# Optimization experiments

Hardware: AMD Instinct MI355X
Metric: run time of the kernel (lower is better)

## Reference

```python
import jax, jax.numpy as jnp
import numpy as np

LATENT = 1024
TEXT = 768
HEADS = 16
HEAD_DIM = LATENT // HEADS
SCALE = HEAD_DIM ** -0.5
LN_EPS = 1e-5


def setup_inputs() -> dict:
    key = jax.random.key(0)
    ks = jax.random.split(key, 16)
    B, Tx, Txf = 4, 4096, 256
    def lin(k, fan_in, fan_out):
        bound = 1.0 / np.sqrt(fan_in)
        kw, kb = jax.random.split(k)
        W = jax.random.uniform(kw, (fan_in, fan_out), jnp.float32, -bound, bound)
        b = jax.random.uniform(kb, (fan_out,), jnp.float32, -bound, bound)
        return W, b
    Wq, bq = lin(ks[0], LATENT, LATENT)
    Wk, bk = lin(ks[1], TEXT, LATENT)
    Wv, bv = lin(ks[2], TEXT, LATENT)
    Wo, bo = lin(ks[3], LATENT, LATENT)
    W1, b1 = lin(ks[4], LATENT, 4 * LATENT)
    W2, b2 = lin(ks[5], 4 * LATENT, LATENT)
    return {
        "x": jax.random.normal(ks[6], (B, Tx, LATENT), jnp.float32),
        "xf": jax.random.normal(ks[7], (B, Txf, TEXT), jnp.float32),
        "Wq": Wq, "bq": bq, "Wk": Wk, "bk": bk, "Wv": Wv, "bv": bv,
        "Wo": Wo, "bo": bo,
        "ln_g": jnp.ones((LATENT,), jnp.float32),
        "ln_b": jnp.zeros((LATENT,), jnp.float32),
        "W1": W1, "b1": b1, "W2": W2, "b2": b2,
    }


def reference(x, xf, Wq, bq, Wk, bk, Wv, bv, Wo, bo, ln_g, ln_b, W1, b1, W2, b2):
    B, Tx, D = x.shape
    Txf = xf.shape[1]
    # projections -> [B, H, T, Dh]
    q = (x @ Wq + bq).reshape(B, Tx, HEADS, HEAD_DIM).transpose(0, 2, 1, 3)
    k = (xf @ Wk + bk).reshape(B, Txf, HEADS, HEAD_DIM).transpose(0, 2, 1, 3)
    v = (xf @ Wv + bv).reshape(B, Txf, HEADS, HEAD_DIM).transpose(0, 2, 1, 3)
    # chunked loop in original == full softmax over keys (dropout=0 at eval)
    scores = jnp.einsum('bhqd,bhkd->bhqk', q * SCALE, k)
    probs = jax.nn.softmax(scores, axis=-1)
    attn = jnp.einsum('bhqk,bhkd->bhqd', probs, v)
    out = attn.transpose(0, 2, 1, 3).reshape(B, Tx, D)
    out = out @ Wo + bo
    # FFN: LayerNorm -> Linear -> GELU(exact) -> Linear
    mu = jnp.mean(out, axis=-1, keepdims=True)
    var = jnp.var(out, axis=-1, keepdims=True)
    h = (out - mu) * jax.lax.rsqrt(var + LN_EPS) * ln_g + ln_b
    h = jax.nn.gelu(h @ W1 + b1, approximate=False)
    ffn = h @ W2 + b2
    out = out + ffn
    return x + out
```

## Files before the change

### kernel.cpp

```cpp
#include <hip/hip_runtime.h>
#include <hip/hip_bf16.h>
#include <cmath>

typedef __bf16 bf16_t;
typedef __bf16 bf16x8 __attribute__((ext_vector_type(8)));
typedef __bf16 bf16x4 __attribute__((ext_vector_type(4)));
typedef float f32x4 __attribute__((ext_vector_type(4)));

#define LATENT 1024
#define HEADS 16
#define HD 64
#define TX 4096
#define TXF 256
#define SCALE_ATTN 0.125f

static __device__ __forceinline__ float b2f(bf16_t b) { return (float)b; }
static __device__ __forceinline__ bf16_t f2b(float f) { return (bf16_t)f; }

static __device__ __forceinline__ void glds16(const bf16_t* g, bf16_t* l) {
    __builtin_amdgcn_global_load_lds(
        (const __attribute__((address_space(1))) void*)g,
        (__attribute__((address_space(3))) void*)l, 16, 0, 0);
}

#define MFMA16(a, b, c) __builtin_amdgcn_mfma_f32_16x16x32_bf16(a, b, c, 0, 0, 0)

__global__ __launch_bounds__(256) void cvt_k(const float* __restrict__ in,
                                             bf16_t* __restrict__ out, long n4) {
    long i = (long)blockIdx.x * 256 + threadIdx.x;
    long stride = (long)gridDim.x * 256;
    for (; i < n4; i += stride) {
        float4 v = ((const float4*)in)[i];
        bf16x4 o;
        o[0] = f2b(v.x); o[1] = f2b(v.y); o[2] = f2b(v.z); o[3] = f2b(v.w);
        *(bf16x4*)&out[i * 4] = o;
    }
}

__global__ __launch_bounds__(256) void tr6_k(
    const float* __restrict__ s0, bf16_t* __restrict__ d0,
    const float* __restrict__ s1, bf16_t* __restrict__ d1,
    const float* __restrict__ s2, bf16_t* __restrict__ d2,
    const float* __restrict__ s3, bf16_t* __restrict__ d3,
    const float* __restrict__ s4, bf16_t* __restrict__ d4,
    const float* __restrict__ s5, bf16_t* __restrict__ d5) {
    int id = blockIdx.x;
    const float* src; bf16_t* dst; int R, C, bx, by;
    if (id < 1024)      { src = s0; dst = d0; R = 1024; C = 1024; bx = id & 31;  by = id >> 5; }
    else if (id < 1792) { id -= 1024; src = s1; dst = d1; R = 768;  C = 1024; bx = id & 31;  by = id >> 5; }
    else if (id < 2560) { id -= 1792; src = s2; dst = d2; R = 768;  C = 1024; bx = id & 31;  by = id >> 5; }
    else if (id < 3584) { id -= 2560; src = s3; dst = d3; R = 1024; C = 1024; bx = id & 31;  by = id >> 5; }
    else if (id < 7680) { id -= 3584; src = s4; dst = d4; R = 1024; C = 4096; bx = id & 127; by = id >> 7; }
    else                { id -= 7680; src = s5; dst = d5; R = 4096; C = 1024; bx = id & 31;  by = id >> 5; }
    __shared__ float t[32][33];
    int x = threadIdx.x & 31, y0 = threadIdx.x >> 5;
    for (int i = 0; i < 32; i += 8)
        t[y0 + i][x] = src[(long)(by * 32 + y0 + i) * C + bx * 32 + x];
    __syncthreads();
    for (int i = 0; i < 32; i += 8)
        dst[(long)(bx * 32 + y0 + i) * R + by * 32 + x] = f2b(t[x][y0 + i]);
}

template <int EPI>
__global__ __launch_bounds__(256, 2) void gemm_k(
    const bf16_t* __restrict__ A, const bf16_t* __restrict__ Bt,
    const float* __restrict__ bias, void* __restrict__ C,
    const bf16_t* __restrict__ resb16, const float* __restrict__ resf32,
    int M, int N, int K) {
    __shared__ __align__(16) bf16_t As[128 * 64];
    __shared__ __align__(16) bf16_t Bs[128 * 64];
    int tid = threadIdx.x;
    int lane = tid & 63, wid = tid >> 6;
    int quad = lane >> 4, l16 = lane & 15;
    int wm = wid >> 1, wn = wid & 1;
    int srow0 = wid * 8 + (lane >> 3);
    int schunk = (lane & 7) ^ (lane >> 3);

    int nwg = gridDim.x * gridDim.y;
    int wgid = blockIdx.y * gridDim.x + blockIdx.x;
    int cpx = nwg >> 3;
    int swz = (wgid & 7) * cpx + (wgid >> 3);
    long bm = swz % gridDim.x;
    long bn = swz / gridDim.x;

    f32x4 acc[4][4] = {};
    const bf16_t* Ab = A + (bm * 128 + srow0) * (long)K + schunk * 8;
    const bf16_t* Bb = Bt + (bn * 128 + srow0) * (long)K + schunk * 8;
    bf16_t* AsD = As + wid * 512;
    bf16_t* BsD = Bs + wid * 512;

    for (int k0 = 0; k0 < K; k0 += 64) {
        __syncthreads();
#pragma unroll
        for (int t = 0; t < 4; t++) {
            glds16(Ab + k0 + (long)t * 32 * K, AsD + t * 2048);
            glds16(Bb + k0 + (long)t * 32 * K, BsD + t * 2048);
        }
        __syncthreads();
#pragma unroll
        for (int s = 0; s < 2; s++) {
            bf16x8 af[4], bfr[4];
#pragma unroll
            for (int mi = 0; mi < 4; mi++) {
                int r = wm * 64 + mi * 16 + l16;
                af[mi] = *(const bf16x8*)&As[r * 64 + (((s * 4 + quad) ^ (r & 7)) * 8)];
            }
#pragma unroll
            for (int ni = 0; ni < 4; ni++) {
                int r = wn * 64 + ni * 16 + l16;
                bfr[ni] = *(const bf16x8*)&Bs[r * 64 + (((s * 4 + quad) ^ (r & 7)) * 8)];
            }
#pragma unroll
            for (int mi = 0; mi < 4; mi++)
#pragma unroll
                for (int ni = 0; ni < 4; ni++)
                    acc[mi][ni] = MFMA16(af[mi], bfr[ni], acc[mi][ni]);
        }
    }

    int colb = (int)bn * 128 + wn * 64;
    float bvv[4];
#pragma unroll
    for (int ni = 0; ni < 4; ni++) bvv[ni] = bias[colb + ni * 16 + l16];
#pragma unroll
    for (int mi = 0; mi < 4; mi++) {
        long grow = bm * 128 + wm * 64 + mi * 16 + quad * 4;
#pragma unroll
        for (int r = 0; r < 4; r++) {
            long ro = (grow + r) * (long)N;
#pragma unroll
            for (int ni = 0; ni < 4; ni++) {
                long idx = ro + colb + ni * 16 + l16;
                float v = acc[mi][ni][r] + bvv[ni];
                if (EPI == 0) {
                    ((bf16_t*)C)[idx] = f2b(v);
                } else if (EPI == 2) {
                    ((bf16_t*)C)[idx] =
                        f2b(0.5f * v * (1.0f + erff(v * 0.70710678118f)));
                } else {
                    ((float*)C)[idx] = v + b2f(resb16[idx]) + resf32[idx];
                }
            }
        }
    }
}

__global__ __launch_bounds__(256, 2) void attn_k(const bf16_t* __restrict__ Q,
                                                 const bf16_t* __restrict__ Kb,
                                                 const bf16_t* __restrict__ Vb,
                                                 bf16_t* __restrict__ Ob) {
    __shared__ __align__(16) bf16_t SM[32768];
    bf16_t* Ks = SM;
    bf16_t* Vt = SM + 16384;
    int tid = threadIdx.x;
    int lane = tid & 63, w = tid >> 6;
    int quad = lane >> 4, l16 = lane & 15;
    int qt = blockIdx.x & 63;
    int bh = blockIdx.x >> 6;
    int b = bh >> 4, h = bh & 15;

    {
        const uint4* ks = (const uint4*)(Kb + ((long)(b * TXF + tid) * LATENT + h * HD));
#pragma unroll
        for (int cc = 0; cc < 8; cc++)
            *(uint4*)&Ks[tid * 64 + ((cc ^ (tid & 7)) * 8)] = ks[cc];
        const uint4* vs = (const uint4*)(Vb + ((long)(b * TXF + tid) * LATENT + h * HD));
#pragma unroll
        for (int cc = 0; cc < 8; cc++) {
            uint4 v = vs[cc];
            const bf16_t* e = (const bf16_t*)&v;
#pragma unroll
            for (int j = 0; j < 8; j++) {
                int d = cc * 8 + j;
                Vt[d * 256 + (((tid >> 3) ^ (d & 7)) * 8) + (tid & 7)] = e[j];
            }
        }
    }
    long qrow = (long)(b * TX + qt * 64 + w * 16 + l16) * LATENT + h * HD;
    bf16x8 aq0 = *(const bf16x8*)(Q + qrow + quad * 8);
    bf16x8 aq1 = *(const bf16x8*)(Q + qrow + 32 + quad * 8);
    __syncthreads();

    f32x4 sacc[16] = {};
#pragma unroll
    for (int ni = 0; ni < 16; ni++) {
        int kr = ni * 16 + l16;
        bf16x8 b0 = *(const bf16x8*)&Ks[kr * 64 + ((quad ^ (kr & 7)) * 8)];
        bf16x8 b1 = *(const bf16x8*)&Ks[kr * 64 + (((4 + quad) ^ (kr & 7)) * 8)];
        sacc[ni] = MFMA16(aq0, b0, sacc[ni]);
        sacc[ni] = MFMA16(aq1, b1, sacc[ni]);
    }
#pragma unroll
    for (int r = 0; r < 4; r++) {
        float m = -3e38f;
#pragma unroll
        for (int ni = 0; ni < 16; ni++) m = fmaxf(m, sacc[ni][r]);
#pragma unroll
        for (int off = 1; off < 16; off <<= 1) m = fmaxf(m, __shfl_xor(m, off, 64));
        float s = 0.f;
#pragma unroll
        for (int ni = 0; ni < 16; ni++) {
            float p = __expf((sacc[ni][r] - m) * SCALE_ATTN);
            sacc[ni][r] = p;
            s += p;
        }
#pragma unroll
        for (int off = 1; off < 16; off <<= 1) s += __shfl_xor(s, off, 64);
        float inv = 1.0f / s;
#pragma unroll
        for (int ni = 0; ni < 16; ni++) sacc[ni][r] *= inv;
    }
    __syncthreads();

    bf16_t* Ps = SM;
#pragma unroll
    for (int r = 0; r < 4; r++) {
        int row = w * 16 + quad * 4 + r;
#pragma unroll
        for (int ni = 0; ni < 16; ni++) {
            int col = ni * 16 + l16;
            Ps[row * 256 + (((col >> 3) ^ (row & 7)) * 8) + (col & 7)] =
                f2b(sacc[ni][r]);
        }
    }
    __syncthreads();

    f32x4 oacc[4] = {};
#pragma unroll
    for (int s = 0; s < 8; s++) {
        int prow = w * 16 + l16;
        bf16x8 ap = *(const bf16x8*)&Ps[prow * 256 + (((s * 4 + quad) ^ (prow & 7)) * 8)];
#pragma unroll
        for (int ni = 0; ni < 4; ni++) {
            int vr = ni * 16 + l16;
            bf16x8 bv = *(const bf16x8*)&Vt[vr * 256 + (((s * 4 + quad) ^ (vr & 7)) * 8)];
            oacc[ni] = MFMA16(ap, bv, oacc[ni]);
        }
    }
#pragma unroll
    for (int r = 0; r < 4; r++) {
        long orow = (long)(b * TX + qt * 64 + w * 16 + quad * 4 + r) * LATENT + h * HD;
#pragma unroll
        for (int ni = 0; ni < 4; ni++)
            Ob[orow + ni * 16 + l16] = f2b(oacc[ni][r]);
    }
}

__global__ __launch_bounds__(256) void ln_k(const bf16_t* __restrict__ O,
                                            const float* __restrict__ g,
                                            const float* __restrict__ bb,
                                            bf16_t* __restrict__ H) {
    long row = blockIdx.x;
    int c = threadIdx.x * 4;
    bf16x4 v = *(const bf16x4*)(O + row * LATENT + c);
    float vv[4] = {b2f(v[0]), b2f(v[1]), b2f(v[2]), b2f(v[3])};
    float s = vv[0] + vv[1] + vv[2] + vv[3];
    float s2 = vv[0] * vv[0] + vv[1] * vv[1] + vv[2] * vv[2] + vv[3] * vv[3];
#pragma unroll
    for (int off = 1; off < 64; off <<= 1) {
        s += __shfl_xor(s, off, 64);
        s2 += __shfl_xor(s2, off, 64);
    }
    __shared__ float red[8];
    int lane = threadIdx.x & 63, w = threadIdx.x >> 6;
    if (lane == 0) { red[w] = s; red[w + 4] = s2; }
    __syncthreads();
    s = red[0] + red[1] + red[2] + red[3];
    s2 = red[4] + red[5] + red[6] + red[7];
    float mu = s * (1.0f / 1024.0f);
    float var = s2 * (1.0f / 1024.0f) - mu * mu;
    float rstd = rsqrtf(var + 1e-5f);
    bf16_t* out = H + row * LATENT + c;
#pragma unroll
    for (int j = 0; j < 4; j++)
        out[j] = f2b((vv[j] - mu) * rstd * g[c + j] + bb[c + j]);
}

extern "C" void kernel_launch(void* const* d_in, const int* in_sizes, int n_in,
                              void* d_out, int out_size, void* d_ws,
                              size_t ws_size, hipStream_t stream) {
    const float* x = (const float*)d_in[0];
    const float* xf = (const float*)d_in[1];
    const float* Wq = (const float*)d_in[2];
    const float* bq = (const float*)d_in[3];
    const float* Wk = (const float*)d_in[4];
    const float* bk = (const float*)d_in[5];
    const float* Wv = (const float*)d_in[6];
    const float* bv = (const float*)d_in[7];
    const float* Wo = (const float*)d_in[8];
    const float* bo = (const float*)d_in[9];
    const float* lng = (const float*)d_in[10];
    const float* lnb = (const float*)d_in[11];
    const float* W1 = (const float*)d_in[12];
    const float* b1 = (const float*)d_in[13];
    const float* W2 = (const float*)d_in[14];
    const float* b2 = (const float*)d_in[15];

    char* ws = (char*)d_ws;
    size_t off = 0;
    auto alloc = [&](size_t bytes) {
        void* p = ws + off;
        off += (bytes + 255) & ~(size_t)255;
        return p;
    };
    bf16_t* WqT = (bf16_t*)alloc((size_t)1024 * 1024 * 2);
    bf16_t* WkT = (bf16_t*)alloc((size_t)1024 * 768 * 2);
    bf16_t* WvT = (bf16_t*)alloc((size_t)1024 * 768 * 2);
    bf16_t* WoT = (bf16_t*)alloc((size_t)1024 * 1024 * 2);
    bf16_t* W1T = (bf16_t*)alloc((size_t)4096 * 1024 * 2);
    bf16_t* W2T = (bf16_t*)alloc((size_t)1024 * 4096 * 2);
    bf16_t* Obuf = (bf16_t*)alloc((size_t)16384 * 1024 * 2);
    bf16_t* Hbuf = (bf16_t*)alloc((size_t)16384 * 1024 * 2);
    size_t transient0 = off;
    bf16_t* xc = (bf16_t*)alloc((size_t)16384 * 1024 * 2);
    bf16_t* xfc = (bf16_t*)alloc((size_t)1024 * 768 * 2);
    bf16_t* Qbuf = (bf16_t*)alloc((size_t)16384 * 1024 * 2);
    bf16_t* Kbuf = (bf16_t*)alloc((size_t)1024 * 1024 * 2);
    bf16_t* Vbuf = (bf16_t*)alloc((size_t)1024 * 1024 * 2);
    bf16_t* Abuf = (bf16_t*)alloc((size_t)16384 * 1024 * 2);
    bf16_t* H1 = (bf16_t*)(ws + transient0);

    dim3 blk(256);
    cvt_k<<<dim3(4096), blk, 0, stream>>>(x, xc, (long)16384 * 1024 / 4);
    cvt_k<<<dim3(768), blk, 0, stream>>>(xf, xfc, (long)1024 * 768 / 4);
    tr6_k<<<dim3(11776), blk, 0, stream>>>(Wq, WqT, Wk, WkT, Wv, WvT,
                                           Wo, WoT, W1, W1T, W2, W2T);

    gemm_k<0><<<dim3(128, 8), blk, 0, stream>>>(xc, WqT, bq, Qbuf, nullptr, nullptr, 16384, 1024, 1024);
    gemm_k<0><<<dim3(8, 8), blk, 0, stream>>>(xfc, WkT, bk, Kbuf, nullptr, nullptr, 1024, 1024, 768);
    gemm_k<0><<<dim3(8, 8), blk, 0, stream>>>(xfc, WvT, bv, Vbuf, nullptr, nullptr, 1024, 1024, 768);
    attn_k<<<dim3(4096), blk, 0, stream>>>(Qbuf, Kbuf, Vbuf, Abuf);
    gemm_k<0><<<dim3(128, 8), blk, 0, stream>>>(Abuf, WoT, bo, Obuf, nullptr, nullptr, 16384, 1024, 1024);
    ln_k<<<dim3(16384), blk, 0, stream>>>(Obuf, lng, lnb, Hbuf);
    gemm_k<2><<<dim3(128, 32), blk, 0, stream>>>(Hbuf, W1T, b1, H1, nullptr, nullptr, 16384, 4096, 1024);
    gemm_k<3><<<dim3(128, 8), blk, 0, stream>>>(H1, W2T, b2, d_out, Obuf, x, 16384, 1024, 4096);
}
```

Measured before the change: 732.8 us.

## Switch GEMM inner loop to 32x32x16 MFMA and drop workgroup swizzle

Replaces the 16x16x32 bf16 MFMA tiling (4x4 accumulators per wave) with 32x32x16 MFMA (2x2 accumulators of 16 floats), rewriting the LDS fragment loads and the epilogue's row/column mapping to match. Larger MFMA tiles mean fewer instructions and fewer LDS reads per unit of work. The change also removes the XCD-aware workgroup-id swizzle and uses blockIdx directly, which can hurt L2 locality across chiplets. Epilogue stores now come as 32-wide column runs per row.

```diff
diff --git a/kernel.cpp b/kernel.cpp
--- a/kernel.cpp
+++ b/kernel.cpp
@@ -6,6 +6,7 @@
 typedef __bf16 bf16x8 __attribute__((ext_vector_type(8)));
 typedef __bf16 bf16x4 __attribute__((ext_vector_type(4)));
 typedef float f32x4 __attribute__((ext_vector_type(4)));
+typedef float f32x16 __attribute__((ext_vector_type(16)));
 
 #define LATENT 1024
 #define HEADS 16
@@ -24,6 +25,7 @@
 }
 
 #define MFMA16(a, b, c) __builtin_amdgcn_mfma_f32_16x16x32_bf16(a, b, c, 0, 0, 0)
+#define MFMA32(a, b, c) __builtin_amdgcn_mfma_f32_32x32x16_bf16(a, b, c, 0, 0, 0)
 
 __global__ __launch_bounds__(256) void cvt_k(const float* __restrict__ in,
                                              bf16_t* __restrict__ out, long n4) {
@@ -71,24 +73,21 @@
     __shared__ __align__(16) bf16_t Bs[128 * 64];
     int tid = threadIdx.x;
     int lane = tid & 63, wid = tid >> 6;
-    int quad = lane >> 4, l16 = lane & 15;
+    int l32 = lane & 31, hi = lane >> 5;
     int wm = wid >> 1, wn = wid & 1;
     int srow0 = wid * 8 + (lane >> 3);
     int schunk = (lane & 7) ^ (lane >> 3);
 
-    int nwg = gridDim.x * gridDim.y;
-    int wgid = blockIdx.y * gridDim.x + blockIdx.x;
-    int cpx = nwg >> 3;
-    int swz = (wgid & 7) * cpx + (wgid >> 3);
-    long bm = swz % gridDim.x;
-    long bn = swz / gridDim.x;
-
-    f32x4 acc[4][4] = {};
+    f32x16 acc[2][2] = {};
+    long bm = blockIdx.x, bn = blockIdx.y;
     const bf16_t* Ab = A + (bm * 128 + srow0) * (long)K + schunk * 8;
     const bf16_t* Bb = Bt + (bn * 128 + srow0) * (long)K + schunk * 8;
     bf16_t* AsD = As + wid * 512;
     bf16_t* BsD = Bs + wid * 512;
 
+    int ra0 = wm * 64 + l32, ra1 = wm * 64 + 32 + l32;
+    int rb0 = wn * 64 + l32, rb1 = wn * 64 + 32 + l32;
+
     for (int k0 = 0; k0 < K; k0 += 64) {
         __syncthreads();
 #pragma unroll
@@ -98,40 +97,41 @@
         }
         __syncthreads();
 #pragma unroll
-        for (int s = 0; s < 2; s++) {
-            bf16x8 af[4], bfr[4];
-#pragma unroll
-            for (int mi = 0; mi < 4; mi++) {
-                int r = wm * 64 + mi * 16 + l16;
-                af[mi] = *(const bf16x8*)&As[r * 64 + (((s * 4 + quad) ^ (r & 7)) * 8)];
+        for (int kp = 0; kp < 2; kp++) {
+            bf16x8 af[2][2], bfr[2][2];
+#pragma unroll
+            for (int ks = 0; ks < 2; ks++) {
+                int ch = (kp * 2 + ks) * 2 + hi;
+                af[0][ks] = *(const bf16x8*)&As[ra0 * 64 + ((ch ^ (ra0 & 7)) * 8)];
+                af[1][ks] = *(const bf16x8*)&As[ra1 * 64 + ((ch ^ (ra1 & 7)) * 8)];
+                bfr[0][ks] = *(const bf16x8*)&Bs[rb0 * 64 + ((ch ^ (rb0 & 7)) * 8)];
+                bfr[1][ks] = *(const bf16x8*)&Bs[rb1 * 64 + ((ch ^ (rb1 & 7)) * 8)];
             }
 #pragma unroll
-            for (int ni = 0; ni < 4; ni++) {
-                int r = wn * 64 + ni * 16 + l16;
-                bfr[ni] = *(const bf16x8*)&Bs[r * 64 + (((s * 4 + quad) ^ (r & 7)) * 8)];
-            }
-#pragma unroll
-            for (int mi = 0; mi < 4; mi++)
-#pragma unroll
-                for (int ni = 0; ni < 4; ni++)
-                    acc[mi][ni] = MFMA16(af[mi], bfr[ni], acc[mi][ni]);
+            for (int ks = 0; ks < 2; ks++)
+#pragma unroll
+                for (int mi = 0; mi < 2; mi++)
+#pragma unroll
+                    for (int ni = 0; ni < 2; ni++)
+                        acc[mi][ni] = MFMA32(af[mi][ks], bfr[ni][ks], acc[mi][ni]);
         }
     }
 
     int colb = (int)bn * 128 + wn * 64;
-    float bvv[4];
-#pragma unroll
-    for (int ni = 0; ni < 4; ni++) bvv[ni] = bias[colb + ni * 16 + l16];
-#pragma unroll
-    for (int mi = 0; mi < 4; mi++) {
-        long grow = bm * 128 + wm * 64 + mi * 16 + quad * 4;
-#pragma unroll
-        for (int r = 0; r < 4; r++) {
-            long ro = (grow + r) * (long)N;
-#pragma unroll
-            for (int ni = 0; ni < 4; ni++) {
-                long idx = ro + colb + ni * 16 + l16;
-                float v = acc[mi][ni][r] + bvv[ni];
+    float bvv[2];
+    bvv[0] = bias[colb + l32];
+    bvv[1] = bias[colb + 32 + l32];
+#pragma unroll
+    for (int mi = 0; mi < 2; mi++) {
+#pragma unroll
+        for (int reg = 0; reg < 16; reg++) {
+            long grow = bm * 128 + wm * 64 + mi * 32 +
+                        (reg & 3) + 8 * (reg >> 2) + 4 * hi;
+            long ro = grow * (long)N;
+#pragma unroll
+            for (int ni = 0; ni < 2; ni++) {
+                long idx = ro + colb + ni * 32 + l32;
+                float v = acc[mi][ni][reg] + bvv[ni];
                 if (EPI == 0) {
                     ((bf16_t*)C)[idx] = f2b(v);
                 } else if (EPI == 2) {
```

New measurement: 709.3 us. -3.2%, faster.
